# Kernel tuning notes

Measured on AMD Instinct MI355X. Metric: run time of the kernel, lower is better.

## Reference

```python
import jax, jax.numpy as jnp
import numpy as np

H = 16          # n_head
N = 64          # head_size
LN_EPS = 1e-5 * 8.0 ** 2  # eps * head_size_divisor**2


def _group_norm(x, w, b):
    # x: (B*T, C), H groups of size N, biased variance (torch GroupNorm)
    BT, C = x.shape
    xg = x.reshape(BT, H, C // H)
    m = xg.mean(-1, keepdims=True)
    v = xg.var(-1, keepdims=True)
    xn = (xg - m) / jnp.sqrt(v + LN_EPS)
    return xn.reshape(BT, C) * w + b


def _rwkv7(r, w, k, v, a, b):
    # RWKV-7: S_t = S_{t-1} * diag(exp(-exp(w_t))) + (S_{t-1} a_t) b_t^T + v_t k_t^T ; y_t = S_t r_t
    B, T, C = r.shape
    def rs(z):
        return z.reshape(B, T, H, N).transpose(1, 0, 2, 3)  # (T,B,H,N)
    wd = jnp.exp(-jnp.exp(rs(w)))
    xs = (rs(r), wd, rs(k), rs(v), rs(a), rs(b))
    def step(S, inp):
        rt, wt, kt, vt, at, bt = inp  # each (B,H,N)
        sa = jnp.einsum('bhij,bhj->bhi', S, at)
        S = S * wt[:, :, None, :] + sa[..., None] * bt[:, :, None, :] + vt[..., None] * kt[:, :, None, :]
        return S, jnp.einsum('bhij,bhj->bhi', S, rt)
    S0 = jnp.zeros((B, H, N, N), r.dtype)
    _, y = jax.lax.scan(step, S0, xs)
    return y.transpose(1, 0, 2, 3).reshape(B, T, C)


def setup_inputs():
    key = jax.random.key(0)
    B, T, C = 2, 2048, 1024
    ks = iter(jax.random.split(key, 32))
    def p(shape, s):
        return jax.random.normal(next(ks), shape, jnp.float32) * s
    return {
        'x': p((B, T, C), 1.0),
        'time_maa_x': p((1, 1, C), 0.5), 'time_maa_r': p((1, 1, C), 0.5),
        'time_maa_w': p((1, 1, C), 0.5), 'time_maa_k': p((1, 1, C), 0.5),
        'time_maa_v': p((1, 1, C), 0.5), 'time_maa_a': p((1, 1, C), 0.5),
        'time_maa_g': p((1, 1, C), 0.5),
        'time_decay': p((1, 1, C), 1.0),
        'time_faaaa': p((H, N), 0.1),
        'time_aaaaa': p((1, 1, C), 0.1),
        'time_maa_w1': p((C, 192), 0.02), 'time_maa_w2': p((6, 32, C), 0.02),
        'time_decay_w1': p((C, 64), 0.02), 'time_decay_w2': p((64, C), 0.1),
        'time_aaa_w1': p((C, 64), 0.02), 'time_aaa_w2': p((64, C), 0.1),
        'time_kkk_w1': p((C, 64), 0.02), 'time_kkk_w2': p((64, C), 0.1),
        'gate_w1': p((C, 128), 0.02), 'gate_w2': p((128, C), 0.1),
        'W_r': p((C, C), 0.03), 'W_k': p((C, C), 0.03),
        'W_v': p((C, C), 0.03), 'W_o': p((C, C), 0.03),
        'ln_w': jnp.ones((C,), jnp.float32), 'ln_b': jnp.zeros((C,), jnp.float32),
    }


def reference(x, time_maa_x, time_maa_r, time_maa_w, time_maa_k, time_maa_v,
              time_maa_a, time_maa_g, time_decay, time_faaaa, time_aaaaa,
              time_maa_w1, time_maa_w2, time_decay_w1, time_decay_w2,
              time_aaa_w1, time_aaa_w2, time_kkk_w1, time_kkk_w2,
              gate_w1, gate_w2, W_r, W_k, W_v, W_o, ln_w, ln_b):
    B, T, C = x.shape
    # time_shift: xx[t] = x[t-1] - x[t], x[-1] = 0
    xx = jnp.pad(x, ((0, 0), (1, 0), (0, 0)))[:, :T] - x
    # low-rank token-mix interpolation coefficients (6 branches)
    mix = jnp.tanh((x + xx * time_maa_x) @ time_maa_w1).reshape(B, T, 6, -1)
    m = jnp.einsum('btsd,sdc->sbtc', mix, time_maa_w2)  # (6,B,T,C)
    mr, mw, mk, mv, ma, mg = m[0], m[1], m[2], m[3], m[4], m[5]
    xr = x + xx * (time_maa_r + mr)
    xw = x + xx * (time_maa_w + mw)
    xk = x + xx * (time_maa_k + mk)
    xv = x + xx * (time_maa_v + mv)
    xa = x + xx * (time_maa_a + ma)
    xg = x + xx * (time_maa_g + mg)
    r = xr @ W_r
    w = -jax.nn.softplus(-(time_decay + jnp.tanh(xw @ time_decay_w1) @ time_decay_w2)) - 0.5
    k = xk @ W_k
    v = xv @ W_v
    g = jnp.tanh(xg @ gate_w1) @ gate_w2
    kk = k + jnp.tanh(xk @ time_kkk_w1) @ time_kkk_w2
    kk = kk / jnp.maximum(jnp.linalg.norm(kk, axis=-1, keepdims=True), 1e-12)
    a = jax.nn.sigmoid(time_aaaaa + (xa @ time_aaa_w1) @ time_aaa_w2) * 2.0
    k = k * jnp.exp(jnp.minimum(w * 0.5, 0.0))
    y = _rwkv7(r, w, k, v, -kk, kk * a)
    y = _group_norm(y.reshape(B * T, C), ln_w, ln_b).reshape(B, T, C)
    rh = r.reshape(B, T, H, N)
    kh = k.reshape(B, T, H, N)
    vh = v.reshape(B, T, H, N)
    bonus = ((rh * kh * time_faaaa).sum(-1, keepdims=True) * vh).reshape(B, T, C)
    y = y + bonus
    return (y * g) @ W_o
```

## Files before the change

### kernel.cpp

```cpp
#include <hip/hip_runtime.h>
#include <hip/hip_bf16.h>

using bf16 = __hip_bfloat16;
using bf16x8 = __attribute__((ext_vector_type(8))) short;
using f32x4 = __attribute__((ext_vector_type(4))) float;

#define B_ 2
#define T_ 2048
#define C_ 1024
#define BT_ (B_*T_)
#define H_ 16
#define N_ 64
#define LCH 32
#define NCH (T_/LCH)
#define CHD (B_*H_*NCH)

__device__ __forceinline__ float allred64(float v) {
#pragma unroll
  for (int m = 1; m < 64; m <<= 1) v += __shfl_xor(v, m, 64);
  return v;
}

__device__ __forceinline__ bf16 tobf(float f) { return __float2bfloat16(f); }
__device__ __forceinline__ float frombf(bf16 b) { return __bfloat162float(b); }
__device__ __forceinline__ float bf2f(unsigned short u) {
  unsigned int x = ((unsigned int)u) << 16;
  return __builtin_bit_cast(float, x);
}
__device__ __forceinline__ unsigned short bfbits(float f) {
  return __builtin_bit_cast(unsigned short, __float2bfloat16(f));
}
__device__ __forceinline__ float rdlane(float v, int m) {
  return __builtin_bit_cast(float,
      __builtin_amdgcn_readlane(__builtin_bit_cast(int, v), m));
}

__device__ __forceinline__ f32x4 mfma16x16x32(bf16x8 a, bf16x8 b, f32x4 c) {
  return __builtin_amdgcn_mfma_f32_16x16x32_bf16(a, b, c, 0, 0, 0);
}

typedef const __attribute__((address_space(1))) unsigned int* gas_ptr;
typedef __attribute__((address_space(3))) unsigned int* las_ptr;
__device__ __forceinline__ void gload16(const void* g, void* l) {
  __builtin_amdgcn_global_load_lds((gas_ptr)g, (las_ptr)l, 16, 0, 0);
}

__global__ void ws_diag(float a, float b, float* out) { out[0] = a; out[1] = b; }

struct PrepArgs {
  const float* src[19];
  bf16* dst[19];
};
__constant__ int kTR[19] = {1024,1024,1024,1024, 1024, 32,32,32,32,32,32,
                            1024,64, 1024,64, 1024,64, 1024,128};
__constant__ int kTC[19] = {1024,1024,1024,1024, 192, 1024,1024,1024,1024,1024,1024,
                            64,1024, 64,1024, 64,1024, 128,1024};

__global__ __launch_bounds__(256) void prep_weights(PrepArgs pa) {
  const int job = blockIdx.y;
  const int R = kTR[job], Cc = kTC[job];
  const int ntx = Cc >> 5, nty = R >> 5;
  const int tile = blockIdx.x;
  if (tile >= ntx * nty) return;
  const int tx = tile % ntx, ty = tile / ntx;
  const float* __restrict__ src = pa.src[job];
  bf16* __restrict__ dst = pa.dst[job];
  __shared__ float tl[32][33];
  const int lx = threadIdx.x & 31, ly = threadIdx.x >> 5;
#pragma unroll
  for (int q = 0; q < 4; ++q)
    tl[ly + 8*q][lx] = src[(size_t)(ty*32 + ly + 8*q) * Cc + tx*32 + lx];
  __syncthreads();
#pragma unroll
  for (int q = 0; q < 4; ++q)
    dst[(size_t)(tx*32 + ly + 8*q) * R + ty*32 + lx] = tobf(tl[lx][ly + 8*q]);
}

template<int EPI>
__global__ __launch_bounds__(256) void gemm_bt(
    const bf16* __restrict__ A, int lda,
    const bf16* __restrict__ Bt, int ldb,
    void* __restrict__ Cout, int ldc, int K)
{
  __shared__ short As[64][40];
  __shared__ short Bs[64][40];
  const int bm0 = blockIdx.x * 64;
  const int bn0 = blockIdx.y * 64;
  const int tid = threadIdx.x;
  const int wave = tid >> 6, lane = tid & 63;
  const int lm = lane & 15, kg = lane >> 4;
  const int srow = tid >> 2, scol = (tid & 3) * 8;
  f32x4 acc[4] = {};
  const size_t abase = (size_t)(bm0 + srow) * lda + scol;
  const size_t bbase = (size_t)(bn0 + srow) * ldb + scol;
  for (int k0 = 0; k0 < K; k0 += 32) {
    *(uint4*)&As[srow][scol] = *(const uint4*)(A + abase + k0);
    *(uint4*)&Bs[srow][scol] = *(const uint4*)(Bt + bbase + k0);
    __syncthreads();
    bf16x8 af = *(const bf16x8*)&As[wave*16 + lm][kg*8];
#pragma unroll
    for (int f = 0; f < 4; ++f) {
      bf16x8 bfr = *(const bf16x8*)&Bs[f*16 + lm][kg*8];
      acc[f] = mfma16x16x32(af, bfr, acc[f]);
    }
    __syncthreads();
  }
  const int row0 = bm0 + wave*16 + kg*4;
  const int col0 = bn0 + lm;
#pragma unroll
  for (int f = 0; f < 4; ++f) {
#pragma unroll
    for (int q = 0; q < 4; ++q) {
      float val = acc[f][q];
      size_t o = (size_t)(row0 + q) * ldc + col0 + f*16;
      if (EPI == 0)      ((float*)Cout)[o] = val;
      else if (EPI == 1) ((bf16*)Cout)[o] = tobf(tanhf(val));
      else               ((bf16*)Cout)[o] = tobf(val);
    }
  }
}

struct Proj4Args { const bf16* A[4]; const bf16* Bt[4]; bf16* out[4];
                   int N[4]; int tnh[4]; };
__global__ __launch_bounds__(256) void proj4(Proj4Args p4) {
  const int z = blockIdx.z;
  const int Nn = p4.N[z];
  const int bn0 = blockIdx.y * 64;
  if (bn0 >= Nn) return;
  __shared__ short As[64][40];
  __shared__ short Bs[64][40];
  const bf16* __restrict__ A  = p4.A[z];
  const bf16* __restrict__ Bt = p4.Bt[z];
  bf16* __restrict__ out = p4.out[z];
  const int tnh = p4.tnh[z];
  const int bm0 = blockIdx.x * 64;
  const int tid = threadIdx.x;
  const int wave = tid >> 6, lane = tid & 63;
  const int lm = lane & 15, kg = lane >> 4;
  const int srow = tid >> 2, scol = (tid & 3) * 8;
  f32x4 acc[4] = {};
  const size_t abase = (size_t)(bm0 + srow) * C_ + scol;
  const size_t bbase = (size_t)(bn0 + srow) * C_ + scol;
  for (int k0 = 0; k0 < C_; k0 += 32) {
    *(uint4*)&As[srow][scol] = *(const uint4*)(A + abase + k0);
    *(uint4*)&Bs[srow][scol] = *(const uint4*)(Bt + bbase + k0);
    __syncthreads();
    bf16x8 af = *(const bf16x8*)&As[wave*16 + lm][kg*8];
#pragma unroll
    for (int f = 0; f < 4; ++f) {
      bf16x8 bfr = *(const bf16x8*)&Bs[f*16 + lm][kg*8];
      acc[f] = mfma16x16x32(af, bfr, acc[f]);
    }
    __syncthreads();
  }
  const int row0 = bm0 + wave*16 + kg*4;
  const int col0 = bn0 + lm;
#pragma unroll
  for (int f = 0; f < 4; ++f) {
#pragma unroll
    for (int q = 0; q < 4; ++q) {
      float val = acc[f][q];
      size_t o = (size_t)(row0 + q) * Nn + col0 + f*16;
      out[o] = tobf(tnh ? tanhf(val) : val);
    }
  }
}

template<int EPI>
__global__ __launch_bounds__(256) void gemm128(
    const bf16* __restrict__ A, int lda,
    const bf16* __restrict__ Bt, int ldb,
    void* __restrict__ Cout, int ldc, int K,
    const float* __restrict__ aux1, bf16* __restrict__ aux2)
{
  __shared__ bf16 As[128][32];
  __shared__ bf16 Bs[128][32];
  const int bm0 = blockIdx.x * 128, bn0 = blockIdx.y * 128;
  const int tid = threadIdx.x, wv = tid >> 6, ln = tid & 63;
  const int wr = wv >> 1, wc = wv & 1;
  const int lm = ln & 15, kg = ln >> 4;
  const int srow = ln >> 2, scol = (ln & 3) * 8;
  f32x4 acc[4][4] = {};
  for (int k0 = 0; k0 < K; k0 += 32) {
#pragma unroll
    for (int i = 0; i < 2; ++i) {
      const int r0 = wv*32 + i*16;
      gload16(A  + (size_t)(bm0 + r0 + srow) * lda + k0 + scol, &As[r0][0]);
      gload16(Bt + (size_t)(bn0 + r0 + srow) * ldb + k0 + scol, &Bs[r0][0]);
    }
    asm volatile("s_waitcnt vmcnt(0)" ::: "memory");
    __syncthreads();
    bf16x8 af[4], bfr[4];
#pragma unroll
    for (int m = 0; m < 4; ++m) af[m] = *(const bf16x8*)&As[wr*64 + m*16 + lm][kg*8];
#pragma unroll
    for (int n = 0; n < 4; ++n) bfr[n] = *(const bf16x8*)&Bs[wc*64 + n*16 + lm][kg*8];
#pragma unroll
    for (int m = 0; m < 4; ++m)
#pragma unroll
      for (int n = 0; n < 4; ++n)
        acc[m][n] = mfma16x16x32(af[m], bfr[n], acc[m][n]);
    __syncthreads();
  }
#pragma unroll
  for (int m = 0; m < 4; ++m) {
    const int row0 = bm0 + wr*64 + m*16 + kg*4;
#pragma unroll
    for (int n = 0; n < 4; ++n) {
      const int col = bn0 + wc*64 + n*16 + lm;
#pragma unroll
      for (int q = 0; q < 4; ++q) {
        float val = acc[m][n][q];
        size_t o = (size_t)(row0 + q) * ldc + col;
        if (EPI == 0)      ((float*)Cout)[o] = val;
        else if (EPI == 2) ((bf16*)Cout)[o] = tobf(val);
        else if (EPI == 3) {
          float wr2 = val + aux1[col];
          float sp = fmaxf(-wr2, 0.f) + log1pf(expf(-fabsf(wr2)));
          float w = -sp - 0.5f;
          ((bf16*)Cout)[o] = tobf(-expf(w));
          aux2[o] = tobf(frombf(aux2[o]) * expf(fminf(0.5f*w, 0.f)));
        } else if (EPI == 4) {
          float z = aux1[col] + val;
          ((bf16*)Cout)[o] = tobf(2.f / (1.f + expf(-z)));
        }
      }
    }
  }
}

struct RkvArgs { const bf16* A[3]; const bf16* Bt[3]; bf16* Cq[3]; };
__global__ __launch_bounds__(256) void gemm128_rkv(RkvArgs ra) {
  __shared__ bf16 As[128][32];
  __shared__ bf16 Bs[128][32];
  const bf16* __restrict__ A  = ra.A[blockIdx.z];
  const bf16* __restrict__ Bt = ra.Bt[blockIdx.z];
  bf16* __restrict__ Cout = ra.Cq[blockIdx.z];
  const int bm0 = blockIdx.x * 128, bn0 = blockIdx.y * 128;
  const int tid = threadIdx.x, wv = tid >> 6, ln = tid & 63;
  const int wr = wv >> 1, wc = wv & 1;
  const int lm = ln & 15, kg = ln >> 4;
  const int srow = ln >> 2, scol = (ln & 3) * 8;
  f32x4 acc[4][4] = {};
  for (int k0 = 0; k0 < C_; k0 += 32) {
#pragma unroll
    for (int i = 0; i < 2; ++i) {
      const int r0 = wv*32 + i*16;
      gload16(A  + (size_t)(bm0 + r0 + srow) * C_ + k0 + scol, &As[r0][0]);
      gload16(Bt + (size_t)(bn0 + r0 + srow) * C_ + k0 + scol, &Bs[r0][0]);
    }
    asm volatile("s_waitcnt vmcnt(0)" ::: "memory");
    __syncthreads();
    bf16x8 af[4], bfr[4];
#pragma unroll
    for (int m = 0; m < 4; ++m) af[m] = *(const bf16x8*)&As[wr*64 + m*16 + lm][kg*8];
#pragma unroll
    for (int n = 0; n < 4; ++n) bfr[n] = *(const bf16x8*)&Bs[wc*64 + n*16 + lm][kg*8];
#pragma unroll
    for (int m = 0; m < 4; ++m)
#pragma unroll
      for (int n = 0; n < 4; ++n)
        acc[m][n] = mfma16x16x32(af[m], bfr[n], acc[m][n]);
    __syncthreads();
  }
#pragma unroll
  for (int m = 0; m < 4; ++m) {
    const int row0 = bm0 + wr*64 + m*16 + kg*4;
#pragma unroll
    for (int n = 0; n < 4; ++n) {
      const int col = bn0 + wc*64 + n*16 + lm;
#pragma unroll
      for (int q = 0; q < 4; ++q)
        Cout[(size_t)(row0 + q) * C_ + col] = tobf(acc[m][n][q]);
    }
  }
}

struct Mix6Args { const float* maa[6]; bf16* out[6]; };

__global__ __launch_bounds__(256) void mix_combine(
    const bf16* __restrict__ mixb, const bf16* __restrict__ w2t,
    const float* __restrict__ x, Mix6Args ma)
{
  __shared__ short As[64][40];
  __shared__ short Bs[64][40];
  const int s6 = blockIdx.z;
  const bf16* __restrict__ A  = mixb + s6*32;
  const bf16* __restrict__ Bt = w2t + (size_t)s6*C_*32;
  const float* __restrict__ maa = ma.maa[s6];
  bf16* __restrict__ out = ma.out[s6];
  const int bm0 = blockIdx.x * 64, bn0 = blockIdx.y * 64;
  const int tid = threadIdx.x, wave = tid >> 6, lane = tid & 63;
  const int lm = lane & 15, kg = lane >> 4;
  const int srow = tid >> 2, scol = (tid & 3) * 8;
  *(uint4*)&As[srow][scol] = *(const uint4*)(A + (size_t)(bm0 + srow)*192 + scol);
  *(uint4*)&Bs[srow][scol] = *(const uint4*)(Bt + (size_t)(bn0 + srow)*32 + scol);
  __syncthreads();
  bf16x8 af = *(const bf16x8*)&As[wave*16 + lm][kg*8];
  f32x4 acc[4] = {};
#pragma unroll
  for (int f = 0; f < 4; ++f) {
    bf16x8 bfr = *(const bf16x8*)&Bs[f*16 + lm][kg*8];
    acc[f] = mfma16x16x32(af, bfr, acc[f]);
  }
  const int row0 = bm0 + wave*16 + kg*4;
  const int col0 = bn0 + lm;
#pragma unroll
  for (int f = 0; f < 4; ++f) {
#pragma unroll
    for (int q = 0; q < 4; ++q) {
      const int row = row0 + q, col = col0 + f*16;
      const size_t o = (size_t)row * C_ + col;
      float xv = x[o];
      float xp = (row & (T_ - 1)) ? x[o - C_] : 0.f;
      out[o] = tobf(xv + (xp - xv) * (maa[col] + acc[f][q]));
    }
  }
}

__global__ __launch_bounds__(256) void xin_k(
    const float* __restrict__ x, const float* __restrict__ maa_x,
    bf16* __restrict__ xinb)
{
  size_t idx = (size_t)blockIdx.x * 256 + threadIdx.x;
  int c = idx & (C_ - 1);
  int t = (int)((idx >> 10) & (T_ - 1));
  float xv = x[idx];
  float xp = t ? x[idx - C_] : 0.f;
  xinb[idx] = tobf(xv + (xp - xv) * maa_x[c]);
}

__global__ __launch_bounds__(256) void kk_normalize(
    const bf16* __restrict__ kraw, const float* __restrict__ kkadd,
    bf16* __restrict__ kkout)
{
  const int bt = blockIdx.x;
  const int tid = threadIdx.x;
  const size_t o = (size_t)bt * C_;
  float vals[4]; float ss = 0.f;
#pragma unroll
  for (int q = 0; q < 4; ++q) {
    float u = frombf(kraw[o + tid + q*256]) + kkadd[o + tid + q*256];
    vals[q] = u; ss += u * u;
  }
  ss = allred64(ss);
  __shared__ float red[4];
  const int wave = tid >> 6, lane = tid & 63;
  if (lane == 0) red[wave] = ss;
  __syncthreads();
  float tot = red[0] + red[1] + red[2] + red[3];
  float inv = 1.f / fmaxf(sqrtf(tot), 1e-12f);
#pragma unroll
  for (int q = 0; q < 4; ++q) kkout[o + tid + q*256] = tobf(vals[q] * inv);
}


__global__ __launch_bounds__(256, 2) void rwkv_chunk_pre(
    const bf16* __restrict__ rr, const bf16* __restrict__ lw,
    const bf16* __restrict__ kk_s, const bf16* __restrict__ kkv,
    const bf16* __restrict__ aam, const bf16* __restrict__ vv,
    bf16* __restrict__ wbufb, bf16* __restrict__ sabufb,
    bf16* __restrict__ abybufb, bf16* __restrict__ ckybufb,
    bf16* __restrict__ ubufP, bf16* __restrict__ mbufT)
{
  __shared__ float Am[LCH][33], Cm[LCH][33];
  __shared__ float wtot[4][64];
  __shared__ float lcl[64];
  __shared__ bf16 aCb[LCH][72], rCb[LCH][72], bTb[LCH][72], kTb[LCH][72], vLb[LCH][72];
  __shared__ bf16 bTT[64][40], kTT[64][40], vLT[64][40];
  __shared__ bf16 WT[64][40], SAT[64][40];

  const int ch = blockIdx.x;
  const int c  = ch & (NCH - 1);
  const int bh = ch >> 6;
  const int b  = bh >> 4, h = bh & 15;
  const int tid = threadIdx.x, wv = tid >> 6, ln = tid & 63;
  const int lm = ln & 15, kg = ln >> 4;
  const size_t base = ((size_t)(b*T_ + c*LCH) * C_) + h*N_ + ln;

  float lwr[8], lcE[8];
  {
    float run = 0.f;
#pragma unroll
    for (int q = 0; q < 8; ++q) {
      lwr[q] = frombf(lw[base + (size_t)(wv*8 + q) * C_]);
      lcE[q] = run; run += lwr[q];
    }
    wtot[wv][ln] = run;
  }
  __syncthreads();
  {
    float pre = 0.f;
    for (int w2 = 0; w2 < wv; ++w2) pre += wtot[w2][ln];
    if (wv == 0) lcl[ln] = wtot[0][ln] + wtot[1][ln] + wtot[2][ln] + wtot[3][ln];
#pragma unroll
    for (int q = 0; q < 8; ++q) lcE[q] += pre;
  }
#pragma unroll
  for (int q = 0; q < 8; ++q) {
    const int s = wv*8 + q;
    const size_t off = base + (size_t)s * C_;
    float kkx = frombf(kkv[off]), aax = frombf(aam[off]);
    float kx = frombf(kk_s[off]), rx = frombf(rr[off]);
    float lcI = lcE[q] + lwr[q];
    float eIm = __expf(-lcI);
    float av = -kkx * __expf(lcE[q]);
    float bv = kkx * aax * eIm;
    float kv2 = kx * eIm;
    float rv = rx * __expf(lcI);
    bf16 vxb = vv[off];
    aCb[s][ln] = tobf(av);  rCb[s][ln] = tobf(rv);
    bTb[s][ln] = tobf(bv);  kTb[s][ln] = tobf(kv2);
    vLb[s][ln] = vxb;
    bTT[ln][s] = tobf(bv);  kTT[ln][s] = tobf(kv2);  vLT[ln][s] = vxb;
  }
  __syncthreads();

  {
    const bf16 (*Ab)[72] = (wv < 2) ? aCb : rCb;
    const bf16 (*Bb)[72] = (wv & 1) ? kTb : bTb;
#pragma unroll
    for (int mt = 0; mt < 2; ++mt)
#pragma unroll
      for (int nt = 0; nt < 2; ++nt) {
        f32x4 acc = {};
#pragma unroll
        for (int ks = 0; ks < 2; ++ks) {
          bf16x8 af = *(const bf16x8*)&Ab[mt*16 + lm][ks*32 + kg*8];
          bf16x8 bq = *(const bf16x8*)&Bb[nt*16 + lm][ks*32 + kg*8];
          acc = mfma16x16x32(af, bq, acc);
        }
        const int row0 = mt*16 + kg*4, col = nt*16 + lm;
#pragma unroll
        for (int q = 0; q < 4; ++q) {
          float v = acc[q];
          if (wv == 0)      Am[row0+q][col] = v;
          else if (wv == 1) Cm[row0+q][col] = v;
          else {
            bf16 bv2 = tobf(col <= row0+q ? v : 0.f);
            if (wv == 2) abybufb[(size_t)ch*1024 + (row0+q)*32 + col] = bv2;
            else         ckybufb[(size_t)ch*1024 + (row0+q)*32 + col] = bv2;
          }
        }
      }
  }
  __syncthreads();

  if (wv < 2) {
    float Xr[32], amr[32];
#pragma unroll
    for (int s = 0; s < 32; ++s) amr[s] = Am[s][ln & 31];
    if (wv == 0) {
#pragma unroll
      for (int s = 0; s < 32; ++s) Xr[s] = frombf(aCb[s][ln]);
    } else {
      float cmr[32];
#pragma unroll
      for (int s = 0; s < 32; ++s) cmr[s] = Cm[s][ln & 31];
#pragma unroll
      for (int s = 0; s < 32; ++s) Xr[s] = 0.f;
#pragma unroll
      for (int u = 0; u < 31; ++u) {
        float v = frombf(vLb[u][ln]);
#pragma unroll
        for (int s = u + 1; s < 32; ++s) Xr[s] += rdlane(cmr[s], u) * v;
      }
    }
#pragma unroll
    for (int s = 1; s < 32; ++s) {
      float acc = Xr[s];
#pragma unroll
      for (int u = 0; u < s; ++u) acc += rdlane(amr[s], u) * Xr[u];
      Xr[s] = acc;
    }
    if (wv == 0) {
#pragma unroll
      for (int s = 0; s < 32; ++s) {
        bf16 bv = tobf(Xr[s]);
        WT[ln][s] = bv;
        wbufb[(size_t)ch*2048 + s*64 + ln] = bv;
      }
    } else {
#pragma unroll
      for (int s = 0; s < 32; ++s) {
        bf16 bv = tobf(Xr[s]);
        SAT[ln][s] = bv;
        sabufb[(size_t)ch*2048 + s*64 + ln] = bv;
      }
    }
  }
  __syncthreads();

  {
    const int mt = wv;
    bf16x8 aS = *(const bf16x8*)&SAT[mt*16 + lm][kg*8];
    bf16x8 aV = *(const bf16x8*)&vLT[mt*16 + lm][kg*8];
    bf16x8 aW = *(const bf16x8*)&WT[mt*16 + lm][kg*8];
#pragma unroll
    for (int nt = 0; nt < 4; ++nt) {
      bf16x8 bB = *(const bf16x8*)&bTT[nt*16 + lm][kg*8];
      bf16x8 bK = *(const bf16x8*)&kTT[nt*16 + lm][kg*8];
      f32x4 aU = {}, aG = {};
      aU = mfma16x16x32(aS, bB, aU);
      aU = mfma16x16x32(aV, bK, aU);
      aG = mfma16x16x32(aW, bB, aG);
      const int i0r = mt*16 + kg*4, col = nt*16 + lm;
      float dl = __expf(lcl[col]);
      uint2 up;
      up.x = (unsigned int)bfbits(aU[0]*dl) | ((unsigned int)bfbits(aU[1]*dl) << 16);
      up.y = (unsigned int)bfbits(aU[2]*dl) | ((unsigned int)bfbits(aU[3]*dl) << 16);
      *(uint2*)(ubufP + (size_t)ch*4096 + (mt*4 + nt)*256 + ln*4) = up;
      float m0 = (aG[0] + (i0r+0 == col ? 1.f : 0.f)) * dl;
      float m1 = (aG[1] + (i0r+1 == col ? 1.f : 0.f)) * dl;
      float m2 = (aG[2] + (i0r+2 == col ? 1.f : 0.f)) * dl;
      float m3 = (aG[3] + (i0r+3 == col ? 1.f : 0.f)) * dl;
      uint2 mp;
      mp.x = (unsigned int)bfbits(m0) | ((unsigned int)bfbits(m1) << 16);
      mp.y = (unsigned int)bfbits(m2) | ((unsigned int)bfbits(m3) << 16);
      const int laned = (((mt*2) + (kg >> 1)) & 3) * 16 + lm;
      *(uint2*)(mbufT + (size_t)ch*4096 + (nt*2 + (mt >> 1))*512
                + laned*8 + (kg & 1)*4) = mp;
    }
  }
}

__global__ __launch_bounds__(256) void rwkv_chunk_state(
    const bf16* __restrict__ mbufT, const bf16* __restrict__ ubufP,
    bf16* __restrict__ s0bufb)
{
  __shared__ bf16 Sst[4][16][72];
  const int bh = blockIdx.x;
  const int tid = threadIdx.x, wv = tid >> 6, ln = tid & 63;
  const int lm = ln & 15, kg = ln >> 4;

#pragma unroll
  for (int r = 0; r < 16; ++r) {
    Sst[wv][r][ln] = tobf(0.f);
    if (ln < 8) Sst[wv][r][64 + ln] = tobf(0.f);
  }

  bf16x8 BfA[4][2], BfB[4][2];
  uint2 UpA[4], UpB[4];
  auto prefetch = [&](bf16x8 (&Bf)[4][2], uint2 (&Up)[4], int c) {
    const size_t chp = (size_t)(bh*NCH + c) * 4096;
#pragma unroll
    for (int nt = 0; nt < 4; ++nt) {
      Bf[nt][0] = *(const bf16x8*)(mbufT + chp + (nt*2 + 0)*512 + ln*8);
      Bf[nt][1] = *(const bf16x8*)(mbufT + chp + (nt*2 + 1)*512 + ln*8);
      Up[nt]    = *(const uint2*) (ubufP + chp + (wv*4 + nt)*256 + ln*4);
    }
  };
  prefetch(BfA, UpA, 0);
  prefetch(BfB, UpB, 1);

  auto body = [&](bf16x8 (&Bf)[4][2], uint2 (&Up)[4], int c) {
    const size_t ch4 = (size_t)(bh*NCH + c) * 4096;
    const int sr = ln >> 2, sc = (ln & 3) * 16;
    uint4 v0 = *(const uint4*)&Sst[wv][sr][sc];
    uint4 v1 = *(const uint4*)&Sst[wv][sr][sc + 8];
    *(uint4*)(s0bufb + ch4 + (size_t)(wv*16 + sr)*64 + sc) = v0;
    *(uint4*)(s0bufb + ch4 + (size_t)(wv*16 + sr)*64 + sc + 8) = v1;
    bf16x8 A0 = *(const bf16x8*)&Sst[wv][lm][kg*8];
    bf16x8 A1 = *(const bf16x8*)&Sst[wv][lm][32 + kg*8];
    f32x4 acc[4];
#pragma unroll
    for (int nt = 0; nt < 4; ++nt) {
      acc[nt][0] = bf2f((unsigned short)(Up[nt].x & 0xffff));
      acc[nt][1] = bf2f((unsigned short)(Up[nt].x >> 16));
      acc[nt][2] = bf2f((unsigned short)(Up[nt].y & 0xffff));
      acc[nt][3] = bf2f((unsigned short)(Up[nt].y >> 16));
      acc[nt] = mfma16x16x32(A0, Bf[nt][0], acc[nt]);
      acc[nt] = mfma16x16x32(A1, Bf[nt][1], acc[nt]);
    }
    int cp = c + 2; if (cp > NCH - 1) cp = NCH - 1;
    prefetch(Bf, Up, cp);
#pragma unroll
    for (int nt = 0; nt < 4; ++nt)
#pragma unroll
      for (int q = 0; q < 4; ++q)
        Sst[wv][kg*4 + q][nt*16 + lm] = tobf(acc[nt][q]);
  };

  for (int cc = 0; cc < NCH; cc += 2) {
    body(BfA, UpA, cc);
    body(BfB, UpB, cc + 1);
  }
}

__global__ __launch_bounds__(256, 4) void rwkv_chunk_out(
    const bf16* __restrict__ rr, const bf16* __restrict__ lw,
    const bf16* __restrict__ vv, const bf16* __restrict__ s0bufb,
    const bf16* __restrict__ wbufb, const bf16* __restrict__ sabufb,
    const bf16* __restrict__ abybufb, const bf16* __restrict__ ckybufb,
    float* __restrict__ y)
{
  __shared__ bf16 S0b[64][72];
  __shared__ bf16 Wb[LCH][72], Rlb[LCH][72];
  __shared__ bf16 ABl[LCH][40], CKl[LCH][40];
  __shared__ bf16 SAot[64][40], VlT[64][40];
  __shared__ float wtot[4][64];
  const int ch = blockIdx.x;
  const int c = ch & (NCH - 1), bh = ch >> 6, b = bh >> 4, h = bh & 15;
  const int tid = threadIdx.x, wv = tid >> 6, ln = tid & 63;
  const int lm = ln & 15, kg = ln >> 4;
  const size_t base = ((size_t)(b*T_ + c*LCH) * C_) + h*N_ + ln;

  float lwr[8], lcE[8];
  {
    float run = 0.f;
#pragma unroll
    for (int q = 0; q < 8; ++q) {
      lwr[q] = frombf(lw[base + (size_t)(wv*8 + q) * C_]);
      lcE[q] = run; run += lwr[q];
    }
    wtot[wv][ln] = run;
  }
  __syncthreads();
  {
    float pre = 0.f;
    for (int w2 = 0; w2 < wv; ++w2) pre += wtot[w2][ln];
#pragma unroll
    for (int q = 0; q < 8; ++q) lcE[q] += pre;
  }
#pragma unroll
  for (int q = 0; q < 8; ++q) {
    const int s = wv*8 + q;
    const size_t off = base + (size_t)s * C_;
    Rlb[s][ln] = tobf(frombf(rr[off]) * __expf(lcE[q] + lwr[q]));
    VlT[ln][s] = vv[off];
  }
#pragma unroll
  for (int t = 0; t < 2; ++t) {
    int cc2 = tid*2 + t; int ri = cc2 >> 3, co = (cc2 & 7) * 8;
    *(uint4*)&S0b[ri][co] = *(const uint4*)(s0bufb + (size_t)ch*4096 + ri*64 + co);
  }
  { int ri = tid >> 3, co = (tid & 7) * 8;
    *(uint4*)&Wb[ri][co] = *(const uint4*)(wbufb + (size_t)ch*2048 + ri*64 + co); }
  if (tid < 128) {
    int ri = tid >> 2, co = (tid & 3) * 8;
    *(uint4*)&ABl[ri][co] = *(const uint4*)(abybufb + (size_t)ch*1024 + ri*32 + co);
  } else {
    int t2 = tid - 128; int ri = t2 >> 2, co = (t2 & 3) * 8;
    *(uint4*)&CKl[ri][co] = *(const uint4*)(ckybufb + (size_t)ch*1024 + ri*32 + co);
  }
  __syncthreads();

  const int mt = wv >> 1, ntb = (wv & 1) * 2;
#pragma unroll
  for (int t = 0; t < 2; ++t) {
    const int nt = ntb + t;
    const int row0 = mt*16 + kg*4, col = nt*16 + lm;
    f32x4 acc;
#pragma unroll
    for (int q = 0; q < 4; ++q)
      acc[q] = frombf(sabufb[(size_t)ch*2048 + (row0+q)*64 + col]);
#pragma unroll
    for (int ks = 0; ks < 2; ++ks) {
      bf16x8 af = *(const bf16x8*)&Wb[mt*16 + lm][ks*32 + kg*8];
      bf16x8 bq = *(const bf16x8*)&S0b[nt*16 + lm][ks*32 + kg*8];
      acc = mfma16x16x32(af, bq, acc);
    }
#pragma unroll
    for (int q = 0; q < 4; ++q) SAot[col][row0+q] = tobf(acc[q]);
  }
  __syncthreads();

#pragma unroll
  for (int t = 0; t < 2; ++t) {
    const int nt = ntb + t;
    f32x4 acc = {};
#pragma unroll
    for (int ks = 0; ks < 2; ++ks) {
      bf16x8 af = *(const bf16x8*)&Rlb[mt*16 + lm][ks*32 + kg*8];
      bf16x8 bq = *(const bf16x8*)&S0b[nt*16 + lm][ks*32 + kg*8];
      acc = mfma16x16x32(af, bq, acc);
    }
    {
      bf16x8 af = *(const bf16x8*)&ABl[mt*16 + lm][kg*8];
      bf16x8 bq = *(const bf16x8*)&SAot[nt*16 + lm][kg*8];
      acc = mfma16x16x32(af, bq, acc);
    }
    {
      bf16x8 af = *(const bf16x8*)&CKl[mt*16 + lm][kg*8];
      bf16x8 bq = *(const bf16x8*)&VlT[nt*16 + lm][kg*8];
      acc = mfma16x16x32(af, bq, acc);
    }
    const int row0 = mt*16 + kg*4, col = nt*16 + lm;
#pragma unroll
    for (int q = 0; q < 4; ++q)
      y[((size_t)(b*T_ + c*LCH + row0 + q)) * C_ + h*N_ + col] = acc[q];
  }
}

__global__ __launch_bounds__(256) void gn_bonus_gate(
    const float* __restrict__ y, const bf16* __restrict__ rr,
    const bf16* __restrict__ kk_s, const bf16* __restrict__ vv,
    const bf16* __restrict__ gg, const float* __restrict__ faaaa,
    const float* __restrict__ lnw, const float* __restrict__ lnb,
    bf16* __restrict__ zb)
{
  const int bt = blockIdx.x;
  const int wave = threadIdx.x >> 6, lane = threadIdx.x & 63;
  const float inv64 = 1.f / 64.f;
  for (int h = wave; h < H_; h += 4) {
    const int c = h * 64 + lane;
    const size_t o = (size_t)bt * C_ + c;
    float yv = y[o];
    float mean = allred64(yv) * inv64;
    float d = yv - mean;
    float var = allred64(d * d) * inv64;
    float xn = d * rsqrtf(var + 6.4e-4f);
    float gn = xn * lnw[c] + lnb[c];
    float rk = allred64(frombf(rr[o]) * frombf(kk_s[o]) * faaaa[c]);
    float z = (gn + rk * frombf(vv[o])) * frombf(gg[o]);
    zb[o] = tobf(z);
  }
}

extern "C" void kernel_launch(void* const* d_in, const int* in_sizes, int n_in,
                              void* d_out, int out_size, void* d_ws, size_t ws_size,
                              hipStream_t stream)
{
  const float* x     = (const float*)d_in[0];
  const float* maa_x = (const float*)d_in[1];
  const float* maa_r = (const float*)d_in[2];
  const float* maa_w = (const float*)d_in[3];
  const float* maa_k = (const float*)d_in[4];
  const float* maa_v = (const float*)d_in[5];
  const float* maa_a = (const float*)d_in[6];
  const float* maa_g = (const float*)d_in[7];
  const float* tdec  = (const float*)d_in[8];
  const float* faaaa = (const float*)d_in[9];
  const float* aaaaa = (const float*)d_in[10];
  const float* maa_w1= (const float*)d_in[11];
  const float* maa_w2= (const float*)d_in[12];
  const float* dec_w1= (const float*)d_in[13];
  const float* dec_w2= (const float*)d_in[14];
  const float* aaa_w1= (const float*)d_in[15];
  const float* aaa_w2= (const float*)d_in[16];
  const float* kkk_w1= (const float*)d_in[17];
  const float* kkk_w2= (const float*)d_in[18];
  const float* gate_w1=(const float*)d_in[19];
  const float* gate_w2=(const float*)d_in[20];
  const float* W_r   = (const float*)d_in[21];
  const float* W_k   = (const float*)d_in[22];
  const float* W_v   = (const float*)d_in[23];
  const float* W_o   = (const float*)d_in[24];
  const float* lnw   = (const float*)d_in[25];
  const float* lnb   = (const float*)d_in[26];

  char* ws = (char*)d_ws;
  size_t cur = 0;
  auto alloc = [&](size_t bytes) -> void* {
    void* p = ws + cur; cur += (bytes + 255) & ~(size_t)255; return p;
  };
  const size_t FBT = (size_t)BT_ * C_ * sizeof(float);
  const size_t HBT = (size_t)BT_ * C_ * 2;

  bf16* rb   = (bf16*)alloc(HBT);
  bf16* kb   = (bf16*)alloc(HBT);
  bf16* vb   = (bf16*)alloc(HBT);
  bf16* gbb  = (bf16*)alloc(HBT);
  bf16* WtR  = (bf16*)alloc((size_t)C_*C_*2);
  bf16* WtK  = (bf16*)alloc((size_t)C_*C_*2);
  bf16* WtV  = (bf16*)alloc((size_t)C_*C_*2);
  bf16* WtO  = (bf16*)alloc((size_t)C_*C_*2);
  bf16* w1t  = (bf16*)alloc((size_t)192*C_*2);
  bf16* w2t  = (bf16*)alloc((size_t)6*C_*32*2);
  bf16* d1t  = (bf16*)alloc((size_t)64*C_*2);
  bf16* d2t  = (bf16*)alloc((size_t)C_*64*2);
  bf16* a1t  = (bf16*)alloc((size_t)64*C_*2);
  bf16* a2t  = (bf16*)alloc((size_t)C_*64*2);
  bf16* k1t  = (bf16*)alloc((size_t)64*C_*2);
  bf16* k2t  = (bf16*)alloc((size_t)C_*64*2);
  bf16* g1t  = (bf16*)alloc((size_t)128*C_*2);
  bf16* g2t  = (bf16*)alloc((size_t)C_*128*2);
  bf16* lwb  = (bf16*)alloc(HBT);
  bf16* kkb  = (bf16*)alloc(HBT);
  bf16* aamt = (bf16*)alloc(HBT);
  bf16* s0bufb = kkb;

  const size_t ubase = cur;
  float* mtmp = (float*)alloc(FBT);
  bf16* xinb = (bf16*)alloc(HBT);
  bf16* mixb = (bf16*)alloc((size_t)BT_*192*2);
  bf16* xbr[6];
  for (int s = 0; s < 6; ++s) xbr[s] = (bf16*)alloc(HBT);
  bf16* h64k = (bf16*)alloc((size_t)BT_*64*2);
  bf16* h64d = (bf16*)alloc((size_t)BT_*64*2);
  bf16* h64a = (bf16*)alloc((size_t)BT_*64*2);
  bf16* h128b= (bf16*)alloc((size_t)BT_*128*2);
  const size_t tmp_end = cur;
  cur = ubase;
  bf16*  wbufb   = (bf16*)alloc((size_t)CHD*2048*2);
  bf16*  sabufb  = (bf16*)alloc((size_t)CHD*2048*2);
  bf16*  abybufb = (bf16*)alloc((size_t)CHD*1024*2);
  bf16*  ckybufb = (bf16*)alloc((size_t)CHD*1024*2);
  bf16*  ubufP   = (bf16*)alloc((size_t)CHD*4096*2);
  bf16*  mbufT   = (bf16*)alloc((size_t)CHD*4096*2);
  bf16*  zb      = (bf16*)ubufP;
  if (tmp_end > cur) cur = tmp_end;
  const size_t need = cur;
  (void)in_sizes; (void)n_in; (void)out_size;

  if (ws_size < need) {
    ws_diag<<<1, 1, 0, stream>>>((float)ws_size, (float)need, (float*)d_out);
    return;
  }

  PrepArgs pa;
  pa.src[0] = W_r;  pa.dst[0] = WtR;
  pa.src[1] = W_k;  pa.dst[1] = WtK;
  pa.src[2] = W_v;  pa.dst[2] = WtV;
  pa.src[3] = W_o;  pa.dst[3] = WtO;
  pa.src[4] = maa_w1; pa.dst[4] = w1t;
  for (int s = 0; s < 6; ++s) { pa.src[5+s] = maa_w2 + (size_t)s*32*C_; pa.dst[5+s] = w2t + (size_t)s*C_*32; }
  pa.src[11] = dec_w1; pa.dst[11] = d1t;
  pa.src[12] = dec_w2; pa.dst[12] = d2t;
  pa.src[13] = aaa_w1; pa.dst[13] = a1t;
  pa.src[14] = aaa_w2; pa.dst[14] = a2t;
  pa.src[15] = kkk_w1; pa.dst[15] = k1t;
  pa.src[16] = kkk_w2; pa.dst[16] = k2t;
  pa.src[17] = gate_w1; pa.dst[17] = g1t;
  pa.src[18] = gate_w2; pa.dst[18] = g2t;
  prep_weights<<<dim3(1024, 19), 256, 0, stream>>>(pa);

  const int EW_GRID = (BT_ * C_) / 256;
  xin_k<<<EW_GRID, 256, 0, stream>>>(x, maa_x, xinb);

  gemm_bt<1><<<dim3(64, 3), 256, 0, stream>>>(xinb, C_, w1t, C_, mixb, 192, C_);

  Mix6Args ma;
  ma.maa[0] = maa_r; ma.maa[1] = maa_w; ma.maa[2] = maa_k;
  ma.maa[3] = maa_v; ma.maa[4] = maa_a; ma.maa[5] = maa_g;
  for (int s = 0; s < 6; ++s) ma.out[s] = xbr[s];
  mix_combine<<<dim3(64, 16, 6), 256, 0, stream>>>(mixb, w2t, x, ma);

  RkvArgs ra;
  ra.A[0] = xbr[0]; ra.Bt[0] = WtR; ra.Cq[0] = rb;
  ra.A[1] = xbr[2]; ra.Bt[1] = WtK; ra.Cq[1] = kb;
  ra.A[2] = xbr[3]; ra.Bt[2] = WtV; ra.Cq[2] = vb;
  gemm128_rkv<<<dim3(32, 8, 3), 256, 0, stream>>>(ra);

  Proj4Args p4;
  p4.A[0] = xbr[2]; p4.Bt[0] = k1t; p4.out[0] = h64k; p4.N[0] = 64;  p4.tnh[0] = 1;
  p4.A[1] = xbr[1]; p4.Bt[1] = d1t; p4.out[1] = h64d; p4.N[1] = 64;  p4.tnh[1] = 1;
  p4.A[2] = xbr[4]; p4.Bt[2] = a1t; p4.out[2] = h64a; p4.N[2] = 64;  p4.tnh[2] = 0;
  p4.A[3] = xbr[5]; p4.Bt[3] = g1t; p4.out[3] = h128b; p4.N[3] = 128; p4.tnh[3] = 1;
  proj4<<<dim3(64, 2, 4), 256, 0, stream>>>(p4);

  gemm128<0><<<dim3(32, 8), 256, 0, stream>>>(h64k, 64, k2t, 64, mtmp, C_, 64, nullptr, nullptr);
  kk_normalize<<<BT_, 256, 0, stream>>>(kb, mtmp, kkb);

  gemm128<3><<<dim3(32, 8), 256, 0, stream>>>(h64d, 64, d2t, 64, lwb, C_, 64, tdec, kb);

  gemm128<4><<<dim3(32, 8), 256, 0, stream>>>(h64a, 64, a2t, 64, aamt, C_, 64, aaaaa, nullptr);

  gemm128<2><<<dim3(32, 8), 256, 0, stream>>>(h128b, 128, g2t, 128, gbb, C_, 128, nullptr, nullptr);

  rwkv_chunk_pre<<<CHD, 256, 0, stream>>>(rb, lwb, kb, kkb, aamt, vb,
      wbufb, sabufb, abybufb, ckybufb, ubufP, mbufT);
  rwkv_chunk_state<<<32, 256, 0, stream>>>(mbufT, ubufP, s0bufb);
  rwkv_chunk_out<<<CHD, 256, 0, stream>>>(rb, lwb, vb, s0bufb, wbufb, sabufb,
      abybufb, ckybufb, (float*)d_out);

  gn_bonus_gate<<<BT_, 256, 0, stream>>>((const float*)d_out, rb, kb, vb, gbb,
                                         faaaa, lnw, lnb, zb);

  gemm128<0><<<dim3(32, 8), 256, 0, stream>>>(zb, C_, WtO, C_, d_out, C_, C_, nullptr, nullptr);
}
```

Measured before the change: 329.2 us.

## Use bf16 intermediates for x and kk-add, alias LDS to raise chunk_pre occupancy

xin_k now also writes a bf16 copy of x, and mix_combine reads that copy instead of fp32 x, which halves the bytes it reads across its six-fold re-reads. The kkk projection output becomes bf16 instead of fp32, cutting traffic into kk_normalize. rwkv_chunk_pre shares one LDS buffer between aCb/rCb and WT/SAT, with an extra barrier so the register loads finish before the buffer is overwritten. This lets launch bounds ask for 3 blocks per CU. The cost is some precision loss on x and kk, and possible register spills under the tighter bound.

Result: faster. 320.3 us (-2.7%).

```diff
diff --git a/kernel.cpp b/kernel.cpp
--- a/kernel.cpp
+++ b/kernel.cpp
@@ -280,7 +280,7 @@
 
 __global__ __launch_bounds__(256) void mix_combine(
     const bf16* __restrict__ mixb, const bf16* __restrict__ w2t,
-    const float* __restrict__ x, Mix6Args ma)
+    const bf16* __restrict__ xb, Mix6Args ma)
 {
   __shared__ short As[64][40];
   __shared__ short Bs[64][40];
@@ -311,8 +311,8 @@
     for (int q = 0; q < 4; ++q) {
       const int row = row0 + q, col = col0 + f*16;
       const size_t o = (size_t)row * C_ + col;
-      float xv = x[o];
-      float xp = (row & (T_ - 1)) ? x[o - C_] : 0.f;
+      float xv = frombf(xb[o]);
+      float xp = (row & (T_ - 1)) ? frombf(xb[o - C_]) : 0.f;
       out[o] = tobf(xv + (xp - xv) * (maa[col] + acc[f][q]));
     }
   }
@@ -320,7 +320,7 @@
 
 __global__ __launch_bounds__(256) void xin_k(
     const float* __restrict__ x, const float* __restrict__ maa_x,
-    bf16* __restrict__ xinb)
+    bf16* __restrict__ xinb, bf16* __restrict__ xb)
 {
   size_t idx = (size_t)blockIdx.x * 256 + threadIdx.x;
   int c = idx & (C_ - 1);
@@ -328,10 +328,11 @@
   float xv = x[idx];
   float xp = t ? x[idx - C_] : 0.f;
   xinb[idx] = tobf(xv + (xp - xv) * maa_x[c]);
+  xb[idx] = tobf(xv);
 }
 
 __global__ __launch_bounds__(256) void kk_normalize(
-    const bf16* __restrict__ kraw, const float* __restrict__ kkadd,
+    const bf16* __restrict__ kraw, const bf16* __restrict__ kkadd,
     bf16* __restrict__ kkout)
 {
   const int bt = blockIdx.x;
@@ -340,7 +341,7 @@
   float vals[4]; float ss = 0.f;
 #pragma unroll
   for (int q = 0; q < 4; ++q) {
-    float u = frombf(kraw[o + tid + q*256]) + kkadd[o + tid + q*256];
+    float u = frombf(kraw[o + tid + q*256]) + frombf(kkadd[o + tid + q*256]);
     vals[q] = u; ss += u * u;
   }
   ss = allred64(ss);
@@ -355,7 +356,7 @@
 }
 
 
-__global__ __launch_bounds__(256, 2) void rwkv_chunk_pre(
+__global__ __launch_bounds__(256, 3) void rwkv_chunk_pre(
     const bf16* __restrict__ rr, const bf16* __restrict__ lw,
     const bf16* __restrict__ kk_s, const bf16* __restrict__ kkv,
     const bf16* __restrict__ aam, const bf16* __restrict__ vv,
@@ -366,9 +367,13 @@
   __shared__ float Am[LCH][33], Cm[LCH][33];
   __shared__ float wtot[4][64];
   __shared__ float lcl[64];
-  __shared__ bf16 aCb[LCH][72], rCb[LCH][72], bTb[LCH][72], kTb[LCH][72], vLb[LCH][72];
+  __shared__ bf16 bTb[LCH][72], kTb[LCH][72], vLb[LCH][72];
   __shared__ bf16 bTT[64][40], kTT[64][40], vLT[64][40];
-  __shared__ bf16 WT[64][40], SAT[64][40];
+  __shared__ bf16 uni[5120];
+  bf16 (*aCb)[72] = (bf16(*)[72])uni;
+  bf16 (*rCb)[72] = (bf16(*)[72])(uni + 2304);
+  bf16 (*WT)[40]  = (bf16(*)[40])uni;
+  bf16 (*SAT)[40] = (bf16(*)[40])(uni + 2560);
 
   const int ch = blockIdx.x;
   const int c  = ch & (NCH - 1);
@@ -446,26 +451,28 @@
   }
   __syncthreads();
 
+  float Xr[32], amr[32];
+  if (wv == 0) {
+#pragma unroll
+    for (int s = 0; s < 32; ++s) amr[s] = Am[s][ln & 31];
+#pragma unroll
+    for (int s = 0; s < 32; ++s) Xr[s] = frombf(aCb[s][ln]);
+  } else if (wv == 1) {
+    float cmr[32];
+#pragma unroll
+    for (int s = 0; s < 32; ++s) { amr[s] = Am[s][ln & 31]; cmr[s] = Cm[s][ln & 31]; }
+#pragma unroll
+    for (int s = 0; s < 32; ++s) Xr[s] = 0.f;
+#pragma unroll
+    for (int u = 0; u < 31; ++u) {
+      float v = frombf(vLb[u][ln]);
+#pragma unroll
+      for (int s = u + 1; s < 32; ++s) Xr[s] += rdlane(cmr[s], u) * v;
+    }
+  }
+  __syncthreads();
+
   if (wv < 2) {
-    float Xr[32], amr[32];
-#pragma unroll
-    for (int s = 0; s < 32; ++s) amr[s] = Am[s][ln & 31];
-    if (wv == 0) {
-#pragma unroll
-      for (int s = 0; s < 32; ++s) Xr[s] = frombf(aCb[s][ln]);
-    } else {
-      float cmr[32];
-#pragma unroll
-      for (int s = 0; s < 32; ++s) cmr[s] = Cm[s][ln & 31];
-#pragma unroll
-      for (int s = 0; s < 32; ++s) Xr[s] = 0.f;
-#pragma unroll
-      for (int u = 0; u < 31; ++u) {
-        float v = frombf(vLb[u][ln]);
-#pragma unroll
-        for (int s = u + 1; s < 32; ++s) Xr[s] += rdlane(cmr[s], u) * v;
-      }
-    }
 #pragma unroll
     for (int s = 1; s < 32; ++s) {
       float acc = Xr[s];
@@ -754,7 +761,6 @@
   auto alloc = [&](size_t bytes) -> void* {
     void* p = ws + cur; cur += (bytes + 255) & ~(size_t)255; return p;
   };
-  const size_t FBT = (size_t)BT_ * C_ * sizeof(float);
   const size_t HBT = (size_t)BT_ * C_ * 2;
 
   bf16* rb   = (bf16*)alloc(HBT);
@@ -781,8 +787,9 @@
   bf16* s0bufb = kkb;
 
   const size_t ubase = cur;
-  float* mtmp = (float*)alloc(FBT);
+  bf16* mtmpb = (bf16*)alloc(HBT);
   bf16* xinb = (bf16*)alloc(HBT);
+  bf16* xb   = (bf16*)alloc(HBT);
   bf16* mixb = (bf16*)alloc((size_t)BT_*192*2);
   bf16* xbr[6];
   for (int s = 0; s < 6; ++s) xbr[s] = (bf16*)alloc(HBT);
@@ -826,7 +833,7 @@
   prep_weights<<<dim3(1024, 19), 256, 0, stream>>>(pa);
 
   const int EW_GRID = (BT_ * C_) / 256;
-  xin_k<<<EW_GRID, 256, 0, stream>>>(x, maa_x, xinb);
+  xin_k<<<EW_GRID, 256, 0, stream>>>(x, maa_x, xinb, xb);
 
   gemm_bt<1><<<dim3(64, 3), 256, 0, stream>>>(xinb, C_, w1t, C_, mixb, 192, C_);
 
@@ -834,7 +841,7 @@
   ma.maa[0] = maa_r; ma.maa[1] = maa_w; ma.maa[2] = maa_k;
   ma.maa[3] = maa_v; ma.maa[4] = maa_a; ma.maa[5] = maa_g;
   for (int s = 0; s < 6; ++s) ma.out[s] = xbr[s];
-  mix_combine<<<dim3(64, 16, 6), 256, 0, stream>>>(mixb, w2t, x, ma);
+  mix_combine<<<dim3(64, 16, 6), 256, 0, stream>>>(mixb, w2t, xb, ma);
 
   RkvArgs ra;
   ra.A[0] = xbr[0]; ra.Bt[0] = WtR; ra.Cq[0] = rb;
@@ -849,8 +856,8 @@
   p4.A[3] = xbr[5]; p4.Bt[3] = g1t; p4.out[3] = h128b; p4.N[3] = 128; p4.tnh[3] = 1;
   proj4<<<dim3(64, 2, 4), 256, 0, stream>>>(p4);
 
-  gemm128<0><<<dim3(32, 8), 256, 0, stream>>>(h64k, 64, k2t, 64, mtmp, C_, 64, nullptr, nullptr);
-  kk_normalize<<<BT_, 256, 0, stream>>>(kb, mtmp, kkb);
+  gemm128<2><<<dim3(32, 8), 256, 0, stream>>>(h64k, 64, k2t, 64, mtmpb, C_, 64, nullptr, nullptr);
+  kk_normalize<<<BT_, 256, 0, stream>>>(kb, mtmpb, kkb);
 
   gemm128<3><<<dim3(32, 8), 256, 0, stream>>>(h64d, 64, d2t, 64, lwb, C_, 64, tdec, kb);
 
```
